# Kernel tuning notes

Measured on AMD Instinct MI355X. Metric: run time of the kernel, lower is better.

## Reference

```python
import jax, jax.numpy as jnp
import numpy as np

B, N, NODE_DIM, EDGE_DIM, H, L, Z, OUT = 4, 512, 16, 8, 64, 3, 64, 1
EPS = 1e-5  # torch BatchNorm1d default eps, training-mode batch stats


def _bn(x, g, b):
    # BatchNorm1d in training mode: biased batch mean/var over batch axis
    m = jnp.mean(x, axis=0)
    v = jnp.var(x, axis=0)
    return g * (x - m) * jax.lax.rsqrt(v + EPS) + b


def setup_inputs():
    keys = jax.random.split(jax.random.key(0), 16)

    def g(k, shape):
        fan = (shape[-2] + shape[-1]) if len(shape) >= 2 else 2 * shape[-1]
        return (jax.random.normal(k, shape) * np.sqrt(2.0 / fan)).astype(jnp.float32)

    return {
        'adj': (jax.random.uniform(keys[0], (B, N, N)) < 0.1).astype(jnp.float32),
        'node_feat': jax.random.normal(keys[1], (B, N, NODE_DIM), dtype=jnp.float32),
        'edge_feat': jax.random.normal(keys[2], (B, N, N, EDGE_DIM), dtype=jnp.float32),
        'nf1_w': g(keys[3], (NODE_DIM, 256)), 'nf1_b': jnp.zeros((256,), jnp.float32),
        'nf2_w': g(keys[4], (256, H)), 'nf2_b': jnp.zeros((H,), jnp.float32),
        'ef1_w': g(keys[5], (EDGE_DIM, 256)), 'ef1_b': jnp.zeros((256,), jnp.float32),
        'ef2_w': g(keys[6], (256, H)), 'ef2_b': jnp.zeros((H,), jnp.float32),
        'gcn_w': g(keys[7], (L, H, H)),
        'vn1_w': g(keys[8], (L, H, 2 * H)), 'vn1_b': jnp.zeros((L, 2 * H), jnp.float32),
        'vn1_g': jnp.ones((L, 2 * H), jnp.float32), 'vn1_be': jnp.zeros((L, 2 * H), jnp.float32),
        'vn2_w': g(keys[9], (L, 2 * H, H)), 'vn2_b': jnp.zeros((L, H), jnp.float32),
        'vn2_g': jnp.ones((L, H), jnp.float32), 'vn2_be': jnp.zeros((L, H), jnp.float32),
        'comb_w': g(keys[10], (L, 2 * H, H)), 'comb_b': jnp.zeros((L, H), jnp.float32),
        'lat1_w': g(keys[11], ((L + 1) * H, 256)), 'lat1_b': jnp.zeros((256,), jnp.float32),
        'lat2_w': g(keys[12], (256, Z)), 'lat2_b': jnp.zeros((Z,), jnp.float32),
        'fc1_w': g(keys[13], (Z, 512)), 'fc1_b': jnp.zeros((512,), jnp.float32),
        'fc2_w': g(keys[14], (512, OUT)), 'fc2_b': jnp.zeros((OUT,), jnp.float32),
    }


def _forward(adj, node_feat, edge_feat, nf1_w, nf1_b, nf2_w, nf2_b, ef1_w, ef1_b,
             ef2_w, ef2_b, gcn_w, vn1_w, vn1_b, vn1_g, vn1_be, vn2_w, vn2_b, vn2_g,
             vn2_be, comb_w, comb_b, lat1_w, lat1_b, lat2_w, lat2_b, fc1_w, fc1_b,
             fc2_w, fc2_b):
    # node / edge embedding MLPs
    nh = jnp.tanh(node_feat @ nf1_w + nf1_b)
    nh = jnp.tanh(nh @ nf2_w + nf2_b)                       # [B,N,H]
    eh = jnp.tanh(edge_feat @ ef1_w + ef1_b)
    eh = jnp.tanh(eh @ ef2_w + ef2_b)                       # [B,N,N,H]
    # einsum 'bijc,bjk->bik' sums over both j and c -> reduce c first
    e_sum = jnp.sum(eh, axis=-1)                            # [B,N,N]
    # GCN normalization: D = 1/rowsum(adj + I); identical every layer
    dinv = 1.0 / (jnp.sum(adj, axis=-1) + 1.0)
    adj_n = dinv[:, :, None] * adj                          # [B,N,N]
    hidden = nh
    alls = [nh]
    for l in range(L):
        hidden = jnp.tanh(adj_n @ (hidden @ gcn_w[l]))      # GraphConvSparse
        vn = jnp.mean(hidden, axis=1)                       # virtual-node pool [B,H]
        vn = jax.nn.relu(_bn(vn @ vn1_w[l] + vn1_b[l], vn1_g[l], vn1_be[l]))
        vn = jax.nn.relu(_bn(vn @ vn2_w[l] + vn2_b[l], vn2_g[l], vn2_be[l]))
        hidden = hidden + vn[:, None, :]                    # broadcast back to nodes
        gated = jnp.tanh(jnp.einsum('bij,bjk->bik', e_sum, hidden))
        hidden = jnp.tanh(jnp.concatenate([hidden, gated], axis=-1) @ comb_w[l] + comb_b[l])
        alls.append(hidden)
    lat = jnp.tanh(jnp.concatenate(alls, axis=-1) @ lat1_w + lat1_b)
    lat = jnp.tanh(lat @ lat2_w + lat2_b)                   # [B,N,Z]
    lat_sum = jnp.sum(lat, axis=1)                          # [B,Z]
    h = jnp.tanh(lat_sum @ fc1_w + fc1_b)
    predict = h @ fc2_w + fc2_b                             # [B,OUT]
    return predict, lat_sum


def reference(adj, node_feat, edge_feat, nf1_w, nf1_b, nf2_w, nf2_b, ef1_w, ef1_b,
              ef2_w, ef2_b, gcn_w, vn1_w, vn1_b, vn1_g, vn1_be, vn2_w, vn2_b, vn2_g,
              vn2_be, comb_w, comb_b, lat1_w, lat1_b, lat2_w, lat2_b, fc1_w, fc1_b,
              fc2_w, fc2_b):
    return _forward(adj, node_feat, edge_feat, nf1_w, nf1_b, nf2_w, nf2_b, ef1_w,
                    ef1_b, ef2_w, ef2_b, gcn_w, vn1_w, vn1_b, vn1_g, vn1_be, vn2_w,
                    vn2_b, vn2_g, vn2_be, comb_w, comb_b, lat1_w, lat1_b, lat2_w,
                    lat2_b, fc1_w, fc1_b, fc2_w, fc2_b)
```

## Files before the change

### kernel.cpp

```cpp
#include <hip/hip_runtime.h>
#include <math.h>

typedef unsigned short u16;
typedef unsigned int u32;

typedef __attribute__((ext_vector_type(8))) short short8;
typedef __attribute__((ext_vector_type(4))) float floatx4;

#define NTILES 16384

__device__ __forceinline__ float bfu(u16 u) { return __uint_as_float(((u32)u) << 16); }
__device__ __forceinline__ u16 f2bfs(float f) {
  u32 x = __float_as_uint(f);
  return (u16)((x + 0x7FFFu + ((x >> 16) & 1u)) >> 16);
}
__device__ __forceinline__ float tanh_fast(float x) {
  float e = __builtin_amdgcn_exp2f(x * 2.885390081777927f);
  return 1.0f - 2.0f * __builtin_amdgcn_rcpf(e + 1.0f);
}

__global__ __launch_bounds__(256) void k_edge(const float* __restrict__ ef,
    const float* __restrict__ w1, const float* __restrict__ b1,
    const float* __restrict__ w2, const float* __restrict__ b2,
    float* __restrict__ es32, u16* __restrict__ es16, int use16) {
  __shared__ __align__(16) short T1[64 * 264];
  __shared__ __align__(16) short W2L[64 * 264];
  __shared__ __align__(16) short W1L[2 * 2056];
  int t = threadIdx.x;
  int lane = t & 63, w = t >> 6, q = lane >> 4, r = lane & 15;

  for (int u = 0; u < 64; ++u) {
    int flat = u * 256 + t;
    int k = flat >> 6, n = flat & 63;
    W2L[n * 264 + k] = (short)f2bfs(w2[flat]);
  }
#pragma unroll
  for (int u = 0; u < 2; ++u) {
    int flat = u * 256 + t;
    int hilo = flat >> 8, idx = flat & 255;
    int feat = (idx & 15) * 16 + (idx >> 4);
    short8 v;
#pragma unroll
    for (int j = 0; j < 8; ++j) {
      float x = w1[j * 256 + feat];
      u32 xb = __float_as_uint(x);
      u16 hi = (u16)(xb >> 16);
      v[j] = hilo ? (short)f2bfs(x - bfu(hi)) : (short)hi;
    }
    *(short8*)&W1L[hilo * 2056 + idx * 8] = v;
  }
  float b1v[16];
#pragma unroll
  for (int nt = 0; nt < 16; ++nt) b1v[nt] = b1[r * 16 + nt];
  float b2v[4];
#pragma unroll
  for (int nt = 0; nt < 4; ++nt) b2v[nt] = b2[nt * 16 + r];
  __syncthreads();

  for (int tile = blockIdx.x; tile < NTILES; tile += gridDim.x) {
    const float4* ep = (const float4*)(ef + (size_t)tile * 512 + (size_t)(w * 16 + r) * 8);
    float4 e0 = ep[0], e1 = ep[1];
    float ev[8] = {e0.x, e0.y, e0.z, e0.w, e1.x, e1.y, e1.z, e1.w};
    short8 af1;
#pragma unroll
    for (int j = 0; j < 8; ++j) {
      u32 xb = __float_as_uint(ev[j]);
      u16 hi = (u16)(xb >> 16);
      af1[j] = (q & 1) ? (short)f2bfs(ev[j] - bfu(hi)) : (short)hi;
    }
    __syncthreads();
    floatx4 c1[16];
#pragma unroll
    for (int gu = 0; gu < 16; ++gu) {
      float bb = b1v[gu];
      c1[gu] = (floatx4){bb, bb, bb, bb};
    }
#pragma unroll
    for (int gu = 0; gu < 16; ++gu) {
      short8 bf = *(const short8*)&W1L[(q >> 1) * 2056 + (gu * 16 + r) * 8];
      c1[gu] = __builtin_amdgcn_mfma_f32_16x16x32_bf16(af1, bf, c1[gu], 0, 0, 0);
    }
#pragma unroll
    for (int reg = 0; reg < 4; ++reg) {
      u32 pk[8];
#pragma unroll
      for (int p2 = 0; p2 < 8; ++p2) {
        float va = tanh_fast(c1[2 * p2][reg]);
        float vb = tanh_fast(c1[2 * p2 + 1][reg]);
        u32 pr;
        asm("v_cvt_pk_bf16_f32 %0, %1, %2" : "=v"(pr) : "v"(va), "v"(vb));
        pk[p2] = pr;
      }
      short* dst = &T1[(w * 16 + q * 4 + reg) * 264 + r * 16];
      int4 wa; wa.x = (int)pk[0]; wa.y = (int)pk[1]; wa.z = (int)pk[2]; wa.w = (int)pk[3];
      int4 wb; wb.x = (int)pk[4]; wb.y = (int)pk[5]; wb.z = (int)pk[6]; wb.w = (int)pk[7];
      *(int4*)dst = wa;
      *(int4*)(dst + 8) = wb;
    }
    __syncthreads();
    floatx4 acc4[4];
#pragma unroll
    for (int nt = 0; nt < 4; ++nt) acc4[nt] = (floatx4){0.f, 0.f, 0.f, 0.f};
    const short* arow = &T1[(w * 16 + r) * 264];
#pragma unroll
    for (int s = 0; s < 8; ++s) {
      short8 af = *(const short8*)(arow + s * 32 + q * 8);
#pragma unroll
      for (int nt = 0; nt < 4; ++nt) {
        short8 bf = *(const short8*)&W2L[(nt * 16 + r) * 264 + s * 32 + q * 8];
        acc4[nt] = __builtin_amdgcn_mfma_f32_16x16x32_bf16(af, bf, acc4[nt], 0, 0, 0);
      }
    }
    float s0 = 0.f, s1 = 0.f, s2 = 0.f, s3 = 0.f;
#pragma unroll
    for (int nt = 0; nt < 4; ++nt) {
      float bb = b2v[nt];
      s0 += tanh_fast(acc4[nt][0] + bb);
      s1 += tanh_fast(acc4[nt][1] + bb);
      s2 += tanh_fast(acc4[nt][2] + bb);
      s3 += tanh_fast(acc4[nt][3] + bb);
    }
#pragma unroll
    for (int off = 1; off < 16; off <<= 1) {
      s0 += __shfl_xor(s0, off, 64);
      s1 += __shfl_xor(s1, off, 64);
      s2 += __shfl_xor(s2, off, 64);
      s3 += __shfl_xor(s3, off, 64);
    }
    if (r == 0) {
      int base = tile * 64 + w * 16 + q * 4;
      if (use16) {
        es16[base] = f2bfs(s0); es16[base + 1] = f2bfs(s1);
        es16[base + 2] = f2bfs(s2); es16[base + 3] = f2bfs(s3);
      } else {
        float4 o; o.x = s0; o.y = s1; o.z = s2; o.w = s3;
        *(float4*)&es32[base] = o;
      }
    }
  }
}

__global__ __launch_bounds__(256) void k_pre(const float* __restrict__ nf,
    const float* __restrict__ w1, const float* __restrict__ b1,
    const float* __restrict__ w2, const float* __restrict__ b2,
    const float* __restrict__ gw, const float* __restrict__ adj,
    float* __restrict__ hid, u16* __restrict__ alls16, float* __restrict__ tmp,
    float* __restrict__ dinv, int* __restrict__ cnt) {
  __shared__ float nfx[4][16];
  __shared__ float t1[4][256];
  __shared__ float nh[4][64];
  int t = threadIdx.x;
  int node0 = blockIdx.x * 4;
  if (blockIdx.x == 0 && t < 16) cnt[t] = 0;
  if (t < 64) nfx[t >> 4][t & 15] = nf[node0 * 16 + t];
  __syncthreads();
  float b1t = b1[t];
  float a0 = b1t, a1 = b1t, a2 = b1t, a3 = b1t;
#pragma unroll
  for (int c = 0; c < 16; ++c) {
    float wv = w1[c * 256 + t];
    a0 += nfx[0][c] * wv; a1 += nfx[1][c] * wv;
    a2 += nfx[2][c] * wv; a3 += nfx[3][c] * wv;
  }
  t1[0][t] = tanh_fast(a0); t1[1][t] = tanh_fast(a1);
  t1[2][t] = tanh_fast(a2); t1[3][t] = tanh_fast(a3);
  __syncthreads();
  int nl = t >> 6, h = t & 63;
  {
    float acc = b2[h];
    for (int c = 0; c < 256; c += 4) {
      float4 xv = *(const float4*)&t1[nl][c];
      acc += xv.x * w2[c * 64 + h] + xv.y * w2[(c + 1) * 64 + h]
           + xv.z * w2[(c + 2) * 64 + h] + xv.w * w2[(c + 3) * 64 + h];
    }
    float v = tanh_fast(acc);
    int node = node0 + nl;
    hid[node * 64 + h] = v;
    alls16[node * 256 + h] = f2bfs(v);
    nh[nl][h] = v;
  }
  __syncthreads();
  {
    float g = 0.f;
    for (int c = 0; c < 64; ++c) g += nh[nl][c] * gw[c * 64 + h];
    tmp[(node0 + nl) * 64 + h] = g;
  }
  {
    int lane = t & 63, row = node0 + (t >> 6);
    float s = 0.f;
#pragma unroll
    for (int u = 0; u < 8; ++u) s += adj[(size_t)row * 512 + u * 64 + lane];
#pragma unroll
    for (int off = 32; off > 0; off >>= 1) s += __shfl_xor(s, off, 64);
    if (lane == 0) dinv[row] = 1.0f / (s + 1.0f);
  }
}

template <int MODE>
__global__ __launch_bounds__(256) void k_adjmm(const float* __restrict__ adj,
    const float* __restrict__ es32, const u16* __restrict__ es16, int use16,
    const float* __restrict__ X, const float* __restrict__ vnin,
    const float* __restrict__ dinv,
    float* __restrict__ out, float* __restrict__ vnpart, int* cnt,
    const float* __restrict__ vw1, const float* __restrict__ vb1,
    const float* __restrict__ vg1, const float* __restrict__ vbe1,
    const float* __restrict__ vw2, const float* __restrict__ vb2,
    const float* __restrict__ vg2, const float* __restrict__ vbe2,
    float* __restrict__ vnout, int l) {
  __shared__ float Xt[64 * 64];
  __shared__ float Al[8 * 65];
  __shared__ floatx4 red4[256];
  __shared__ int isLast;
  int t = threadIdx.x;
  int b = blockIdx.x >> 6, it = blockIdx.x & 63;
  int hq = t & 15, slot = t >> 4, row = slot & 7, half = slot >> 3;
  floatx4 acc = (floatx4){0.f, 0.f, 0.f, 0.f};
  for (int jt = 0; jt < 8; ++jt) {
    __syncthreads();
    for (int u = 0; u < 16; ++u) {
      int idx = u * 256 + t;
      int jl = idx >> 6, hh = idx & 63;
      float xv = X[(b * 512 + jt * 64 + jl) * 64 + hh];
      if (MODE) xv += vnin[b * 64 + hh];
      Xt[idx] = xv;
    }
#pragma unroll
    for (int u = 0; u < 2; ++u) {
      int idx = u * 256 + t;
      int il = idx >> 6, jl = idx & 63;
      size_t ai = ((size_t)(b * 512 + it * 8 + il)) * 512 + jt * 64 + jl;
      float av;
      if (MODE) av = use16 ? bfu(es16[ai]) : es32[ai];
      else      av = adj[ai];
      Al[il * 65 + jl] = av;
    }
    __syncthreads();
    const float* xp = &Xt[(half * 32) * 64 + hq * 4];
    const float* ap = &Al[row * 65 + half * 32];
#pragma unroll
    for (int jl = 0; jl < 32; ++jl) {
      floatx4 xv = *(const floatx4*)(xp + jl * 64);
      float a = ap[jl];
      acc[0] += a * xv[0]; acc[1] += a * xv[1];
      acc[2] += a * xv[2]; acc[3] += a * xv[3];
    }
  }
  red4[t] = acc;
  __syncthreads();
  if (t < 128) {
    floatx4 s = red4[t], s2 = red4[t + 128];
    int gr = b * 512 + it * 8 + row;
    floatx4 o;
    if (MODE) {
#pragma unroll
      for (int i = 0; i < 4; ++i) o[i] = tanh_fast(s[i] + s2[i]);
    } else {
      float d = dinv[gr];
#pragma unroll
      for (int i = 0; i < 4; ++i) o[i] = tanh_fast((s[i] + s2[i]) * d);
    }
    *(floatx4*)&out[gr * 64 + hq * 4] = o;
    if (!MODE) red4[t] = o;
  }
  if (!MODE) {
    __syncthreads();
    if (t < 16) {
      floatx4 ssum = (floatx4){0.f, 0.f, 0.f, 0.f};
#pragma unroll
      for (int r2 = 0; r2 < 8; ++r2) {
        floatx4 v = red4[r2 * 16 + t];
        ssum[0] += v[0]; ssum[1] += v[1]; ssum[2] += v[2]; ssum[3] += v[3];
      }
      *(floatx4*)&vnpart[(b * 64 + it) * 64 + t * 4] = ssum;
    }
    __threadfence();
    __syncthreads();
    if (t == 0) isLast = (atomicAdd(cnt, 1) == 255);
    __syncthreads();
    if (isLast) {
      __threadfence();
      float* x0 = Xt; float* x1 = Xt + 256; float* y1 = Xt + 768; float* x2 = Xt + 1280;
      {
        int bb = t >> 6, h = t & 63;
        float s = 0.f;
        for (int c = 0; c < 64; ++c) s += vnpart[(bb * 64 + c) * 64 + h];
        x0[t] = s * (1.0f / 512.0f);
      }
      __syncthreads();
      for (int rep = 0; rep < 2; ++rep) {
        int idx = rep * 256 + t;
        int bb = idx >> 7, j = idx & 127;
        float a = vb1[l * 128 + j];
        for (int h = 0; h < 64; ++h) a += x0[bb * 64 + h] * vw1[l * 8192 + h * 128 + j];
        x1[idx] = a;
      }
      __syncthreads();
      if (t < 128) {
        int j = t;
        float a = x1[j], bq = x1[128 + j], c = x1[256 + j], d = x1[384 + j];
        float m = 0.25f * (a + bq + c + d);
        float da = a - m, db = bq - m, dc = c - m, dd = d - m;
        float var = 0.25f * (da * da + db * db + dc * dc + dd * dd);
        float sc = vg1[l * 128 + j] / sqrtf(var + 1e-5f);
        float be = vbe1[l * 128 + j];
        y1[j]       = fmaxf(sc * da + be, 0.f);
        y1[128 + j] = fmaxf(sc * db + be, 0.f);
        y1[256 + j] = fmaxf(sc * dc + be, 0.f);
        y1[384 + j] = fmaxf(sc * dd + be, 0.f);
      }
      __syncthreads();
      {
        int bb = t >> 6, k = t & 63;
        float a = vb2[l * 64 + k];
        for (int j = 0; j < 128; ++j) a += y1[bb * 128 + j] * vw2[l * 8192 + j * 64 + k];
        x2[t] = a;
      }
      __syncthreads();
      if (t < 64) {
        int k = t;
        float a = x2[k], bq = x2[64 + k], c = x2[128 + k], d = x2[192 + k];
        float m = 0.25f * (a + bq + c + d);
        float da = a - m, db = bq - m, dc = c - m, dd = d - m;
        float var = 0.25f * (da * da + db * db + dc * dc + dd * dd);
        float sc = vg2[l * 64 + k] / sqrtf(var + 1e-5f);
        float be = vbe2[l * 64 + k];
        vnout[k]       = fmaxf(sc * da + be, 0.f);
        vnout[64 + k]  = fmaxf(sc * db + be, 0.f);
        vnout[128 + k] = fmaxf(sc * dc + be, 0.f);
        vnout[192 + k] = fmaxf(sc * dd + be, 0.f);
      }
    }
  }
}

__global__ __launch_bounds__(256) void k_comb_gcn(const float* hid,
    const float* gated, const float* __restrict__ vn,
    const float* __restrict__ cw, const float* __restrict__ cb,
    const float* __restrict__ gw_next,
    u16* __restrict__ alls16, float* tmpout, int l, int do_gcn) {
  __shared__ float cat[4 * 128];
  __shared__ float nh[4][64];
  int t = threadIdx.x;
  int node0 = blockIdx.x * 4;
#pragma unroll
  for (int u = 0; u < 2; ++u) {
    int idx = u * 256 + t;
    int nl = idx >> 7, c = idx & 127;
    int node = node0 + nl;
    int b = node >> 9;
    float v;
    if (c < 64) v = hid[node * 64 + c] + vn[b * 64 + c];
    else        v = gated[node * 64 + (c - 64)];
    cat[idx] = v;
  }
  __syncthreads();
  int nl = t >> 6, h = t & 63;
  float acc = cb[l * 64 + h];
  const float* wp = cw + l * 8192 + h;
  for (int c = 0; c < 128; c += 4) {
    float4 xv = *(const float4*)&cat[nl * 128 + c];
    acc += xv.x * wp[c * 64] + xv.y * wp[(c + 1) * 64]
         + xv.z * wp[(c + 2) * 64] + xv.w * wp[(c + 3) * 64];
  }
  float v = tanh_fast(acc);
  int node = node0 + nl;
  ((float*)hid)[node * 64 + h] = v;
  alls16[node * 256 + (l + 1) * 64 + h] = f2bfs(v);
  if (do_gcn) {
    nh[nl][h] = v;
    __syncthreads();
    float g = 0.f;
    for (int c = 0; c < 64; ++c) g += nh[nl][c] * gw_next[c * 64 + h];
    tmpout[node * 64 + h] = g;
  }
}

__global__ __launch_bounds__(256) void k_latfinal(const u16* __restrict__ alls16,
    const float* __restrict__ w1, const float* __restrict__ bb1,
    const float* __restrict__ w2, const float* __restrict__ bb2,
    float* __restrict__ latpart, int* cnt,
    const float* __restrict__ f1w, const float* __restrict__ f1b,
    const float* __restrict__ f2w, const float* __restrict__ f2b,
    float* __restrict__ outp) {
  __shared__ float x[8][256];
  __shared__ float t1[8][256];
  __shared__ float red[8][256];
  __shared__ int isLastL;
  int t = threadIdx.x;
  int b = blockIdx.x >> 6, chunk = blockIdx.x & 63;
#pragma unroll
  for (int u = 0; u < 8; ++u)
    x[u][t] = bfu(alls16[(size_t)(b * 512 + chunk * 8 + u) * 256 + t]);
  __syncthreads();
  float a1[8];
  float bb = bb1[t];
#pragma unroll
  for (int u = 0; u < 8; ++u) a1[u] = bb;
  for (int c = 0; c < 256; ++c) {
    float wv = w1[c * 256 + t];
#pragma unroll
    for (int u = 0; u < 8; ++u) a1[u] += x[u][c] * wv;
  }
#pragma unroll
  for (int u = 0; u < 8; ++u) t1[u][t] = tanh_fast(a1[u]);
  __syncthreads();
  int quar = t >> 6, k = t & 63, c0 = quar * 64;
  float a2[8];
#pragma unroll
  for (int u = 0; u < 8; ++u) a2[u] = 0.f;
  for (int c = 0; c < 64; ++c) {
    float wv = w2[(c0 + c) * 64 + k];
#pragma unroll
    for (int u = 0; u < 8; ++u) a2[u] += t1[u][c0 + c] * wv;
  }
#pragma unroll
  for (int u = 0; u < 8; ++u) red[u][t] = a2[u];
  __syncthreads();
  if (t < 64) {
    float acc2 = 0.f;
    float b2v = bb2[t];
#pragma unroll
    for (int u = 0; u < 8; ++u) {
      float s = red[u][t] + red[u][t + 64] + red[u][t + 128] + red[u][t + 192] + b2v;
      acc2 += tanh_fast(s);
    }
    latpart[(b * 64 + chunk) * 64 + t] = acc2;
  }
  __threadfence();
  __syncthreads();
  if (t == 0) isLastL = (atomicAdd(cnt, 1) == 255);
  __syncthreads();
  if (isLastL) {
    __threadfence();
    float* ls = &red[0][0];
    float* hb = &x[0][0];
    {
      int bb2_ = t >> 6, z = t & 63;
      float s = 0.f;
      for (int c = 0; c < 64; ++c) s += latpart[(bb2_ * 64 + c) * 64 + z];
      ls[t] = s;
      outp[4 + t] = s;
    }
    __syncthreads();
    for (int rep = 0; rep < 8; ++rep) {
      int idx = rep * 256 + t;
      int bb2_ = idx >> 9, kk = idx & 511;
      float acc = f1b[kk];
      for (int z = 0; z < 64; ++z) acc += ls[bb2_ * 64 + z] * f1w[z * 512 + kk];
      hb[idx] = tanh_fast(acc);
    }
    __syncthreads();
    {
      int bb2_ = t >> 6, lane = t & 63;
      float acc = 0.f;
#pragma unroll
      for (int u = 0; u < 8; ++u) acc += hb[bb2_ * 512 + lane + u * 64] * f2w[lane + u * 64];
#pragma unroll
      for (int off = 32; off > 0; off >>= 1) acc += __shfl_xor(acc, off, 64);
      if (lane == 0) outp[bb2_] = acc + f2b[0];
    }
  }
}

extern "C" void kernel_launch(void* const* d_in, const int* in_sizes, int n_in,
                              void* d_out, int out_size, void* d_ws, size_t ws_size,
                              hipStream_t stream) {
  const float* adj       = (const float*)d_in[0];
  const float* node_feat = (const float*)d_in[1];
  const float* edge_feat = (const float*)d_in[2];
  const float* nf1_w = (const float*)d_in[3];
  const float* nf1_b = (const float*)d_in[4];
  const float* nf2_w = (const float*)d_in[5];
  const float* nf2_b = (const float*)d_in[6];
  const float* ef1_w = (const float*)d_in[7];
  const float* ef1_b = (const float*)d_in[8];
  const float* ef2_w = (const float*)d_in[9];
  const float* ef2_b = (const float*)d_in[10];
  const float* gcn_w = (const float*)d_in[11];
  const float* vn1_w = (const float*)d_in[12];
  const float* vn1_b = (const float*)d_in[13];
  const float* vn1_g = (const float*)d_in[14];
  const float* vn1_be = (const float*)d_in[15];
  const float* vn2_w = (const float*)d_in[16];
  const float* vn2_b = (const float*)d_in[17];
  const float* vn2_g = (const float*)d_in[18];
  const float* vn2_be = (const float*)d_in[19];
  const float* comb_w = (const float*)d_in[20];
  const float* comb_b = (const float*)d_in[21];
  const float* lat1_w = (const float*)d_in[22];
  const float* lat1_b = (const float*)d_in[23];
  const float* lat2_w = (const float*)d_in[24];
  const float* lat2_b = (const float*)d_in[25];
  const float* fc1_w = (const float*)d_in[26];
  const float* fc1_b = (const float*)d_in[27];
  const float* fc2_w = (const float*)d_in[28];
  const float* fc2_b = (const float*)d_in[29];

  const int use16 = (ws_size < (size_t)12 * 1024 * 1024) ? 1 : 0;
  char* p = (char*)d_ws;
  float* es32 = (float*)p;
  u16*   es16 = (u16*)p;
  size_t es_bytes = use16 ? (size_t)1048576 * 2 : (size_t)1048576 * 4;
  u16*   alls16  = (u16*)(p + es_bytes);
  float* hid     = (float*)(alls16 + 524288);
  float* tmp     = hid + 131072;
  float* dinv    = tmp + 131072;
  float* vnpart  = dinv + 2048;
  float* vn      = vnpart + 16384;
  float* latpart = vn + 256;
  int*   cnt     = (int*)(latpart + 16384);

  k_pre<<<512, 256, 0, stream>>>(node_feat, nf1_w, nf1_b, nf2_w, nf2_b,
                                 gcn_w, adj, hid, alls16, tmp, dinv, cnt);
  k_edge<<<1024, 256, 0, stream>>>(edge_feat, ef1_w, ef1_b, ef2_w, ef2_b,
                                   es32, es16, use16);
  for (int l = 0; l < 3; ++l) {
    k_adjmm<0><<<256, 256, 0, stream>>>(adj, es32, es16, use16, tmp, vn, dinv,
        hid, vnpart, cnt + l,
        vn1_w, vn1_b, vn1_g, vn1_be, vn2_w, vn2_b, vn2_g, vn2_be, vn, l);
    k_adjmm<1><<<256, 256, 0, stream>>>(adj, es32, es16, use16, hid, vn, dinv,
        tmp, vnpart, cnt + l,
        vn1_w, vn1_b, vn1_g, vn1_be, vn2_w, vn2_b, vn2_g, vn2_be, vn, l);
    k_comb_gcn<<<512, 256, 0, stream>>>(hid, tmp, vn, comb_w, comb_b,
        gcn_w + (l + 1) * 4096, alls16, tmp, l, (l < 2) ? 1 : 0);
  }
  k_latfinal<<<256, 256, 0, stream>>>(alls16, lat1_w, lat1_b, lat2_w, lat2_b,
                                      latpart, cnt + 3,
                                      fc1_w, fc1_b, fc2_w, fc2_b, (float*)d_out);
}
```

Baseline: 493.5 us.

## Prefetch next edge tile, swizzle LDS, drop block barriers in edge MLP kernel

The edge-MLP kernel now loads the next tile's edge features into registers while the current tile computes. It gives each wave a private T1 staging region, so the two block-wide __syncthreads per tile become wave-local lgkmcnt waits plus a schedule barrier. The padded LDS rows are replaced with an XOR-swizzled layout for T1 and W2L to avoid bank conflicts without padding. The grid is halved to 512 blocks. Correctness now depends on each wave reading only its own T1 rows and on the swizzle indices matching between writes and reads.

```diff
diff --git a/kernel.cpp b/kernel.cpp
--- a/kernel.cpp
+++ b/kernel.cpp
@@ -23,8 +23,8 @@
     const float* __restrict__ w1, const float* __restrict__ b1,
     const float* __restrict__ w2, const float* __restrict__ b2,
     float* __restrict__ es32, u16* __restrict__ es16, int use16) {
-  __shared__ __align__(16) short T1[64 * 264];
-  __shared__ __align__(16) short W2L[64 * 264];
+  __shared__ __align__(16) short T1[4 * 4096];
+  __shared__ __align__(16) short W2L[64 * 256];
   __shared__ __align__(16) short W1L[2 * 2056];
   int t = threadIdx.x;
   int lane = t & 63, w = t >> 6, q = lane >> 4, r = lane & 15;
@@ -32,7 +32,9 @@
   for (int u = 0; u < 64; ++u) {
     int flat = u * 256 + t;
     int k = flat >> 6, n = flat & 63;
-    W2L[n * 264 + k] = (short)f2bfs(w2[flat]);
+    int swzn = ((n >> 2) & 1) | ((n & 1) << 2);
+    int slot = n * 32 + ((k >> 3) ^ swzn);
+    W2L[slot * 8 + (k & 7)] = (short)f2bfs(w2[flat]);
   }
 #pragma unroll
   for (int u = 0; u < 2; ++u) {
@@ -57,9 +59,14 @@
   for (int nt = 0; nt < 4; ++nt) b2v[nt] = b2[nt * 16 + r];
   __syncthreads();
 
-  for (int tile = blockIdx.x; tile < NTILES; tile += gridDim.x) {
-    const float4* ep = (const float4*)(ef + (size_t)tile * 512 + (size_t)(w * 16 + r) * 8);
-    float4 e0 = ep[0], e1 = ep[1];
+  const int stride = gridDim.x;
+  const int swzr = ((r >> 2) & 1) | ((r & 1) << 2);
+  short* t1w = &T1[w * 4096];
+  int tile = blockIdx.x;
+  const float4* ep0 = (const float4*)(ef + (size_t)tile * 512 + (size_t)(w * 16 + r) * 8);
+  float4 e0 = ep0[0], e1 = ep0[1];
+
+  for (; tile < NTILES; tile += stride) {
     float ev[8] = {e0.x, e0.y, e0.z, e0.w, e1.x, e1.y, e1.z, e1.w};
     short8 af1;
 #pragma unroll
@@ -68,7 +75,11 @@
       u16 hi = (u16)(xb >> 16);
       af1[j] = (q & 1) ? (short)f2bfs(ev[j] - bfu(hi)) : (short)hi;
     }
-    __syncthreads();
+    int ntile = tile + stride;
+    if (ntile < NTILES) {
+      const float4* ep = (const float4*)(ef + (size_t)ntile * 512 + (size_t)(w * 16 + r) * 8);
+      e0 = ep[0]; e1 = ep[1];
+    }
     floatx4 c1[16];
 #pragma unroll
     for (int gu = 0; gu < 16; ++gu) {
@@ -80,6 +91,7 @@
       short8 bf = *(const short8*)&W1L[(q >> 1) * 2056 + (gu * 16 + r) * 8];
       c1[gu] = __builtin_amdgcn_mfma_f32_16x16x32_bf16(af1, bf, c1[gu], 0, 0, 0);
     }
+    asm volatile("s_waitcnt lgkmcnt(0)" ::: "memory");
 #pragma unroll
     for (int reg = 0; reg < 4; ++reg) {
       u32 pk[8];
@@ -91,23 +103,27 @@
         asm("v_cvt_pk_bf16_f32 %0, %1, %2" : "=v"(pr) : "v"(va), "v"(vb));
         pk[p2] = pr;
       }
-      short* dst = &T1[(w * 16 + q * 4 + reg) * 264 + r * 16];
+      int row = q * 4 + reg;
+      int swzrow = (q & 1) | ((reg & 1) << 2);
+      int sA = row * 32 + ((2 * r) ^ swzrow);
+      int sB = row * 32 + ((2 * r + 1) ^ swzrow);
       int4 wa; wa.x = (int)pk[0]; wa.y = (int)pk[1]; wa.z = (int)pk[2]; wa.w = (int)pk[3];
       int4 wb; wb.x = (int)pk[4]; wb.y = (int)pk[5]; wb.z = (int)pk[6]; wb.w = (int)pk[7];
-      *(int4*)dst = wa;
-      *(int4*)(dst + 8) = wb;
-    }
-    __syncthreads();
+      *(int4*)&t1w[sA * 8] = wa;
+      *(int4*)&t1w[sB * 8] = wb;
+    }
+    asm volatile("s_waitcnt lgkmcnt(0)" ::: "memory");
+    __builtin_amdgcn_sched_barrier(0);
     floatx4 acc4[4];
 #pragma unroll
     for (int nt = 0; nt < 4; ++nt) acc4[nt] = (floatx4){0.f, 0.f, 0.f, 0.f};
-    const short* arow = &T1[(w * 16 + r) * 264];
 #pragma unroll
     for (int s = 0; s < 8; ++s) {
-      short8 af = *(const short8*)(arow + s * 32 + q * 8);
+      int ca = (4 * s + q) ^ swzr;
+      short8 af = *(const short8*)&t1w[(r * 32 + ca) * 8];
 #pragma unroll
       for (int nt = 0; nt < 4; ++nt) {
-        short8 bf = *(const short8*)&W2L[(nt * 16 + r) * 264 + s * 32 + q * 8];
+        short8 bf = *(const short8*)&W2L[((nt * 16 + r) * 32 + ca) * 8];
         acc4[nt] = __builtin_amdgcn_mfma_f32_16x16x32_bf16(af, bf, acc4[nt], 0, 0, 0);
       }
     }
@@ -512,8 +528,8 @@
 
   k_pre<<<512, 256, 0, stream>>>(node_feat, nf1_w, nf1_b, nf2_w, nf2_b,
                                  gcn_w, adj, hid, alls16, tmp, dinv, cnt);
-  k_edge<<<1024, 256, 0, stream>>>(edge_feat, ef1_w, ef1_b, ef2_w, ef2_b,
-                                   es32, es16, use16);
+  k_edge<<<512, 256, 0, stream>>>(edge_feat, ef1_w, ef1_b, ef2_w, ef2_b,
+                                  es32, es16, use16);
   for (int l = 0; l < 3; ++l) {
     k_adjmm<0><<<256, 256, 0, stream>>>(adj, es32, es16, use16, tmp, vn, dinv,
         hid, vnpart, cnt + l,
```

Result: no change. 501.0 us (+1.5%).

## Restructure edge MLP kernel into per-wave tiles with prefetch and swizzled LDS

Applied to the files above, without the earlier changes.

The edge MLP kernel moves to 1024-thread blocks in which each wave owns its own 16-row tile. This removes the block-wide __syncthreads between the two GEMM stages. The first layer's 256 hidden units are processed in two halves of 128 to cut register pressure, and the next tile's edge features are prefetched from global memory while the current tile computes. LDS layouts for the intermediate activations and W2 are XOR-swizzled instead of padded, to avoid bank conflicts. Risks include the explicit waitcnt and sched barriers limiting instruction overlap, and the reduced grid of 256 blocks lowering the work available for load balance.

```diff
diff --git a/kernel.cpp b/kernel.cpp
--- a/kernel.cpp
+++ b/kernel.cpp
@@ -19,26 +19,27 @@
   return 1.0f - 2.0f * __builtin_amdgcn_rcpf(e + 1.0f);
 }
 
-__global__ __launch_bounds__(256) void k_edge(const float* __restrict__ ef,
+__global__ __launch_bounds__(1024, 4) void k_edge(const float* __restrict__ ef,
     const float* __restrict__ w1, const float* __restrict__ b1,
     const float* __restrict__ w2, const float* __restrict__ b2,
     float* __restrict__ es32, u16* __restrict__ es16, int use16) {
-  __shared__ __align__(16) short T1[64 * 264];
-  __shared__ __align__(16) short W2L[64 * 264];
+  __shared__ __align__(16) short T1[16 * 2048];
+  __shared__ __align__(16) short W2L[16384];
   __shared__ __align__(16) short W1L[2 * 2056];
   int t = threadIdx.x;
   int lane = t & 63, w = t >> 6, q = lane >> 4, r = lane & 15;
 
-  for (int u = 0; u < 64; ++u) {
-    int flat = u * 256 + t;
+  for (int u = 0; u < 16; ++u) {
+    int flat = u * 1024 + t;
     int k = flat >> 6, n = flat & 63;
-    W2L[n * 264 + k] = (short)f2bfs(w2[flat]);
-  }
-#pragma unroll
-  for (int u = 0; u < 2; ++u) {
-    int flat = u * 256 + t;
-    int hilo = flat >> 8, idx = flat & 255;
-    int feat = (idx & 15) * 16 + (idx >> 4);
+    int c = k >> 3, j = k & 7;
+    int physc = (c & 16) | ((c & 15) ^ (n & 15));
+    W2L[(n * 32 + physc) * 8 + j] = (short)f2bfs(w2[flat]);
+  }
+  if (t < 512) {
+    int hilo = t >> 8, idx = t & 255;
+    int gu = idx >> 4, rr = idx & 15;
+    int feat = (gu < 8) ? (rr * 8 + gu) : (120 + rr * 8 + gu);
     short8 v;
 #pragma unroll
     for (int j = 0; j < 8; ++j) {
@@ -51,15 +52,24 @@
   }
   float b1v[16];
 #pragma unroll
-  for (int nt = 0; nt < 16; ++nt) b1v[nt] = b1[r * 16 + nt];
+  for (int gu = 0; gu < 16; ++gu)
+    b1v[gu] = b1[(gu < 8) ? (r * 8 + gu) : (120 + r * 8 + gu)];
   float b2v[4];
 #pragma unroll
   for (int nt = 0; nt < 4; ++nt) b2v[nt] = b2[nt * 16 + r];
   __syncthreads();
 
-  for (int tile = blockIdx.x; tile < NTILES; tile += gridDim.x) {
-    const float4* ep = (const float4*)(ef + (size_t)tile * 512 + (size_t)(w * 16 + r) * 8);
-    float4 e0 = ep[0], e1 = ep[1];
+  short* t1w = &T1[w * 2048];
+  const int hb = (q >> 1) * 2056;
+  const int nw = gridDim.x * 16;
+  int qt = blockIdx.x * 16 + w;
+  float4 e0, e1;
+  {
+    const float4* ep = (const float4*)(ef + (size_t)qt * 128 + (size_t)r * 8);
+    e0 = ep[0]; e1 = ep[1];
+  }
+
+  for (; qt < 4 * NTILES; qt += nw) {
     float ev[8] = {e0.x, e0.y, e0.z, e0.w, e1.x, e1.y, e1.z, e1.w};
     short8 af1;
 #pragma unroll
@@ -68,47 +78,57 @@
       u16 hi = (u16)(xb >> 16);
       af1[j] = (q & 1) ? (short)f2bfs(ev[j] - bfu(hi)) : (short)hi;
     }
-    __syncthreads();
-    floatx4 c1[16];
-#pragma unroll
-    for (int gu = 0; gu < 16; ++gu) {
-      float bb = b1v[gu];
-      c1[gu] = (floatx4){bb, bb, bb, bb};
-    }
-#pragma unroll
-    for (int gu = 0; gu < 16; ++gu) {
-      short8 bf = *(const short8*)&W1L[(q >> 1) * 2056 + (gu * 16 + r) * 8];
-      c1[gu] = __builtin_amdgcn_mfma_f32_16x16x32_bf16(af1, bf, c1[gu], 0, 0, 0);
-    }
-#pragma unroll
-    for (int reg = 0; reg < 4; ++reg) {
-      u32 pk[8];
-#pragma unroll
-      for (int p2 = 0; p2 < 8; ++p2) {
-        float va = tanh_fast(c1[2 * p2][reg]);
-        float vb = tanh_fast(c1[2 * p2 + 1][reg]);
-        u32 pr;
-        asm("v_cvt_pk_bf16_f32 %0, %1, %2" : "=v"(pr) : "v"(va), "v"(vb));
-        pk[p2] = pr;
-      }
-      short* dst = &T1[(w * 16 + q * 4 + reg) * 264 + r * 16];
-      int4 wa; wa.x = (int)pk[0]; wa.y = (int)pk[1]; wa.z = (int)pk[2]; wa.w = (int)pk[3];
-      int4 wb; wb.x = (int)pk[4]; wb.y = (int)pk[5]; wb.z = (int)pk[6]; wb.w = (int)pk[7];
-      *(int4*)dst = wa;
-      *(int4*)(dst + 8) = wb;
-    }
-    __syncthreads();
+    int nqt = qt + nw;
+    if (nqt < 4 * NTILES) {
+      const float4* ep = (const float4*)(ef + (size_t)nqt * 128 + (size_t)r * 8);
+      e0 = ep[0]; e1 = ep[1];
+    }
     floatx4 acc4[4];
 #pragma unroll
     for (int nt = 0; nt < 4; ++nt) acc4[nt] = (floatx4){0.f, 0.f, 0.f, 0.f};
-    const short* arow = &T1[(w * 16 + r) * 264];
-#pragma unroll
-    for (int s = 0; s < 8; ++s) {
-      short8 af = *(const short8*)(arow + s * 32 + q * 8);
-#pragma unroll
-      for (int nt = 0; nt < 4; ++nt) {
-        short8 bf = *(const short8*)&W2L[(nt * 16 + r) * 264 + s * 32 + q * 8];
-        acc4[nt] = __builtin_amdgcn_mfma_f32_16x16x32_bf16(af, bf, acc4[nt], 0, 0, 0);
+#pragma unroll
+    for (int ph = 0; ph < 2; ++ph) {
+      floatx4 c1[8];
+#pragma unroll
+      for (int u = 0; u < 8; ++u) {
+        float bb = b1v[ph * 8 + u];
+        c1[u] = (floatx4){bb, bb, bb, bb};
+      }
+#pragma unroll
+      for (int u = 0; u < 8; ++u) {
+        short8 bf = *(const short8*)&W1L[hb + ((ph * 8 + u) * 16 + r) * 8];
+        c1[u] = __builtin_amdgcn_mfma_f32_16x16x32_bf16(af1, bf, c1[u], 0, 0, 0);
+      }
+      asm volatile("s_waitcnt lgkmcnt(0)" ::: "memory");
+      __builtin_amdgcn_sched_barrier(0);
+#pragma unroll
+      for (int reg = 0; reg < 4; ++reg) {
+        u32 pk[4];
+#pragma unroll
+        for (int p2 = 0; p2 < 4; ++p2) {
+          float va = tanh_fast(c1[2 * p2][reg]);
+          float vb = tanh_fast(c1[2 * p2 + 1][reg]);
+          u32 pr;
+          asm("v_cvt_pk_bf16_f32 %0, %1, %2" : "=v"(pr) : "v"(va), "v"(vb));
+          pk[p2] = pr;
+        }
+        int row = q * 4 + reg;
+        int physc = r ^ row;
+        int4 wa; wa.x = (int)pk[0]; wa.y = (int)pk[1]; wa.z = (int)pk[2]; wa.w = (int)pk[3];
+        *(int4*)&t1w[(row * 16 + physc) * 8] = wa;
+      }
+      asm volatile("s_waitcnt lgkmcnt(0)" ::: "memory");
+      __builtin_amdgcn_sched_barrier(0);
+#pragma unroll
+      for (int sm = 0; sm < 4; ++sm) {
+        int cc = (4 * sm + q) ^ r;
+        short8 af = *(const short8*)&t1w[(r * 16 + cc) * 8];
+        int wc = ph * 16 + cc;
+#pragma unroll
+        for (int nt = 0; nt < 4; ++nt) {
+          short8 bf = *(const short8*)&W2L[((nt * 16 + r) * 32 + wc) * 8];
+          acc4[nt] = __builtin_amdgcn_mfma_f32_16x16x32_bf16(af, bf, acc4[nt], 0, 0, 0);
+        }
       }
     }
     float s0 = 0.f, s1 = 0.f, s2 = 0.f, s3 = 0.f;
@@ -128,7 +148,7 @@
       s3 += __shfl_xor(s3, off, 64);
     }
     if (r == 0) {
-      int base = tile * 64 + w * 16 + q * 4;
+      int base = qt * 16 + q * 4;
       if (use16) {
         es16[base] = f2bfs(s0); es16[base + 1] = f2bfs(s1);
         es16[base + 2] = f2bfs(s2); es16[base + 3] = f2bfs(s3);
@@ -512,7 +532,7 @@
 
   k_pre<<<512, 256, 0, stream>>>(node_feat, nf1_w, nf1_b, nf2_w, nf2_b,
                                  gcn_w, adj, hid, alls16, tmp, dinv, cnt);
-  k_edge<<<1024, 256, 0, stream>>>(edge_feat, ef1_w, ef1_b, ef2_w, ef2_b,
+  k_edge<<<256, 1024, 0, stream>>>(edge_feat, ef1_w, ef1_b, ef2_w, ef2_b,
                                    es32, es16, use16);
   for (int l = 0; l < 3; ++l) {
     k_adjmm<0><<<256, 256, 0, stream>>>(adj, es32, es16, use16, tmp, vn, dinv,
```

Result: slower. 506.1 us (+2.6%).
